# Optimization experiments

Hardware: AMD Instinct MI355X
Metric: run time of the kernel (lower is better)

The kernel has to match this reference:

```python
import jax, jax.numpy as jnp
import numpy as np

B, SQ, SK, E, H = 2, 256, 512, 512, 256

def _lin_init(k, fan_in, fan_out):
    return jax.random.normal(k, (fan_in, fan_out), jnp.float32) / np.sqrt(fan_in)

def setup_inputs() -> dict:
    key = jax.random.key(0)
    ks = jax.random.split(key, 16)
    inp = {
        'query': jax.random.normal(ks[0], (B, SQ, E), jnp.float32),
        'key':   jax.random.normal(ks[1], (B, SK, E), jnp.float32),
        # encoders
        'Wqe': _lin_init(ks[2], E, H), 'bqe': jnp.zeros((H,), jnp.float32),
        'Wke': _lin_init(ks[3], E, H), 'bke': jnp.zeros((H,), jnp.float32),
        # importance predictor: Linear(2H,H) x1, Linear(H,H) x2, Linear(H,1)
        'W0': _lin_init(ks[4], 2 * H, H), 'b0': jnp.zeros((H,), jnp.float32),
        'W1': _lin_init(ks[5], H, H),     'b1': jnp.zeros((H,), jnp.float32),
        'W2': _lin_init(ks[6], H, H),     'b2': jnp.zeros((H,), jnp.float32),
        'Wf': _lin_init(ks[7], H, 1),     'bf': jnp.zeros((1,), jnp.float32),
        # variance estimator: Linear(2H,H), Linear(H,1), Softplus
        'Wv1': _lin_init(ks[8], 2 * H, H), 'bv1': jnp.zeros((H,), jnp.float32),
        'Wv2': _lin_init(ks[9], H, 1),     'bv2': jnp.zeros((1,), jnp.float32),
    }
    return inp

def reference(query, key, Wqe, bqe, Wke, bke, W0, b0, W1, b1, W2, b2, Wf, bf, Wv1, bv1, Wv2, bv2):
    # Encoders (dropout is identity at eval): [B,Sq,H] and [B,Sk,H]
    qf = jax.nn.relu(jnp.einsum('bqe,eh->bqh', query, Wqe) + bqe)
    kf = jax.nn.relu(jnp.einsum('bke,eh->bkh', key, Wke) + bke)

    # concat([qf, kf]) @ W == qf @ W[:H] + kf @ W[H:]; avoid materializing the 2H concat
    Hd = qf.shape[-1]
    # importance predictor, layer 0 over all (q,k) pairs -> [B,Sq,Sk,H]
    q_part = jnp.einsum('bqh,hd->bqd', qf, W0[:Hd])
    k_part = jnp.einsum('bkh,hd->bkd', kf, W0[Hd:])
    h = jax.nn.relu(q_part[:, :, None, :] + k_part[:, None, :, :] + b0)
    h = jax.nn.relu(jnp.einsum('bqkh,hd->bqkd', h, W1) + b1)
    h = jax.nn.relu(jnp.einsum('bqkh,hd->bqkd', h, W2) + b2)
    importance_logits = (jnp.einsum('bqkh,ho->bqko', h, Wf) + bf)[..., 0]  # [B,Sq,Sk]

    # variance estimator
    qv = jnp.einsum('bqh,hd->bqd', qf, Wv1[:Hd])
    kv = jnp.einsum('bkh,hd->bkd', kf, Wv1[Hd:])
    v = jax.nn.relu(qv[:, :, None, :] + kv[:, None, :, :] + bv1)
    variance = jax.nn.softplus((jnp.einsum('bqkh,ho->bqko', v, Wv2) + bv2)[..., 0])

    return importance_logits, variance
```

## Files before the change

kernel.cpp:

```cpp
#include <hip/hip_runtime.h>
#include <hip/hip_bf16.h>
#include <math.h>

typedef __attribute__((ext_vector_type(4))) float f32x4;
typedef __attribute__((ext_vector_type(8))) short short8;
typedef __attribute__((ext_vector_type(4))) short short4v;

#define H_DIM 256
#define SQ_DIM 256
#define SK_DIM 512
#define E_DIM 512
#define B_DIM 2

__global__ __launch_bounds__(256) void split_cast(const float* __restrict__ query,
                                                  const float* __restrict__ key,
                                                  __hip_bfloat16* __restrict__ A1)
{
    int gid = blockIdx.x * 256 + threadIdx.x;
    int m  = gid >> 7;
    int kq = gid & 127;
    const float* src = (m < 512) ? query + (size_t)m * 512
                                 : key + (size_t)(m - 512) * 512;
    f32x4 v = *(const f32x4*)(src + kq * 4);
    short4v hv, lv;
    #pragma unroll
    for (int j = 0; j < 4; ++j) {
        __hip_bfloat16 h = __float2bfloat16(v[j]);
        float lf = v[j] - __bfloat162float(h);
        __hip_bfloat16 l = __float2bfloat16(lf);
        hv[j] = __builtin_bit_cast(short, h);
        lv[j] = __builtin_bit_cast(short, l);
    }
    *(short4v*)(A1 + (size_t)m * 1024 + kq * 4) = hv;
    *(short4v*)(A1 + (size_t)m * 1024 + 512 + kq * 4) = lv;
}

__global__ __launch_bounds__(256) void transpose_split(
    const float* __restrict__ Wqe, const float* __restrict__ Wke,
    const float* __restrict__ W0,  const float* __restrict__ Wv1,
    const float* __restrict__ W1,  const float* __restrict__ W2,
    __hip_bfloat16* __restrict__ Benc, __hip_bfloat16* __restrict__ Bproj,
    __hip_bfloat16* __restrict__ W1T,  __hip_bfloat16* __restrict__ W2T)
{
    __shared__ float tile[64][65];
    const float* S = nullptr; __hip_bfloat16* D = nullptr; int KJ = 256;
    bool split = true;
    switch (blockIdx.y) {
        case 0: S = Wqe;             D = Benc;                          KJ = 512; break;
        case 1: S = Wke;             D = Benc + 256 * 1024;             KJ = 512; break;
        case 2: S = W0;              D = Bproj;                         KJ = 256; break;
        case 3: S = Wv1;             D = Bproj + 256 * 512;             KJ = 256; break;
        case 4: S = W0 + 256 * 256;  D = Bproj + 512 * 512;             KJ = 256; break;
        case 5: S = Wv1 + 256 * 256; D = Bproj + 512 * 512 + 256 * 512; KJ = 256; break;
        case 6: S = W1;              D = W1T;  KJ = 256; split = false; break;
        case 7: S = W2;              D = W2T;  KJ = 256; split = false; break;
    }
    const int dstStride = split ? 2 * KJ : KJ;
    const int ntile = 4 * (KJ >> 6);
    const int x = blockIdx.x;
    if (x >= ntile) return;
    const int tx = x & 3, ty = x >> 2;
    const int k0 = ty * 64, n0 = tx * 64;
    const int t = threadIdx.x;
    #pragma unroll
    for (int i = 0; i < 16; ++i) {
        int r = (t >> 6) + i * 4;
        int c = t & 63;
        tile[r][c] = S[(size_t)(k0 + r) * 256 + n0 + c];
    }
    __syncthreads();
    #pragma unroll
    for (int i = 0; i < 16; ++i) {
        int r = (t >> 6) + i * 4;
        int c = t & 63;
        float v = tile[c][r];
        __hip_bfloat16 h = __float2bfloat16(v);
        D[(size_t)(n0 + r) * dstStride + k0 + c] = h;
        if (split) {
            float lf = v - __bfloat162float(h);
            D[(size_t)(n0 + r) * dstStride + KJ + k0 + c] = __float2bfloat16(lf);
        }
    }
}

template<int KD, bool SPLIT_OUT>
__global__ __launch_bounds__(256) void gemm3(
    const __hip_bfloat16* __restrict__ Apl,
    const __hip_bfloat16* __restrict__ B0,
    const __hip_bfloat16* __restrict__ B1,
    const float* __restrict__ bias0, const float* __restrict__ bias1,
    __hip_bfloat16* __restrict__ outS,
    float* __restrict__ outF0, float* __restrict__ outF1)
{
    __shared__ char smem[32768];
    const int t = threadIdx.x, lane = t & 63, wave = t >> 6;
    const int wm = wave >> 1, wn = wave & 1;
    const int m0 = blockIdx.y * 64, n0 = blockIdx.x * 64;
    const __hip_bfloat16* Arow = Apl + (size_t)m0 * (2 * KD);
    const __hip_bfloat16* Brow = ((m0 < 512) ? B0 : B1) + (size_t)n0 * (2 * KD);

    auto stage = [&](int c) {
        char* wb = smem + ((c & 1) << 14);
        const int k0 = c * 32;
        #pragma unroll
        for (int i = 0; i < 4; ++i) {
            int u = wave * 64 + lane + i * 256;
            int r = u >> 2;
            int sl = (u & 3) ^ ((r >> 1) & 3);
            int isB = r >> 7;
            int rr = r & 127;
            const __hip_bfloat16* base = isB ? Brow : Arow;
            const __hip_bfloat16* gp = base + (size_t)(rr >> 1) * (2 * KD)
                                       + (rr & 1) * KD + k0 + sl * 8;
            char* lp = wb + (wave * 64 + i * 256) * 16;
            __builtin_amdgcn_global_load_lds((const void*)gp, (void*)lp, 16, 0, 0);
        }
    };

    stage(0);
    __syncthreads();
    f32x4 acc[2][2];
    #pragma unroll
    for (int i = 0; i < 2; ++i)
        #pragma unroll
        for (int j = 0; j < 2; ++j) acc[i][j] = 0.f;

    const int NCH = KD / 32;
    for (int c = 0; c < NCH; ++c) {
        if (c + 1 < NCH) stage(c + 1);
        const char* wb = smem + ((c & 1) << 14);
        short8 ah[2], al[2];
        #pragma unroll
        for (int nt = 0; nt < 2; ++nt) {
            int n = wn * 32 + nt * 16 + (lane & 15);
            int rh = 128 + 2 * n, rl = rh + 1;
            ah[nt] = *(const short8*)(wb + rh * 64 + (((lane >> 4) ^ ((rh >> 1) & 3)) << 4));
            al[nt] = *(const short8*)(wb + rl * 64 + (((lane >> 4) ^ ((rl >> 1) & 3)) << 4));
        }
        #pragma unroll
        for (int mt = 0; mt < 2; ++mt) {
            int m = wm * 32 + mt * 16 + (lane & 15);
            int rh = 2 * m, rl = rh + 1;
            short8 bh = *(const short8*)(wb + rh * 64 + (((lane >> 4) ^ ((rh >> 1) & 3)) << 4));
            short8 bl = *(const short8*)(wb + rl * 64 + (((lane >> 4) ^ ((rl >> 1) & 3)) << 4));
            #pragma unroll
            for (int nt = 0; nt < 2; ++nt) {
                acc[mt][nt] = __builtin_amdgcn_mfma_f32_16x16x32_bf16(ah[nt], bh, acc[mt][nt], 0, 0, 0);
                acc[mt][nt] = __builtin_amdgcn_mfma_f32_16x16x32_bf16(al[nt], bh, acc[mt][nt], 0, 0, 0);
                acc[mt][nt] = __builtin_amdgcn_mfma_f32_16x16x32_bf16(ah[nt], bl, acc[mt][nt], 0, 0, 0);
            }
        }
        __syncthreads();
    }

    #pragma unroll
    for (int mt = 0; mt < 2; ++mt) {
        int m = m0 + wm * 32 + mt * 16 + (lane & 15);
        #pragma unroll
        for (int nt = 0; nt < 2; ++nt) {
            int nb = n0 + wn * 32 + nt * 16 + ((lane >> 4) << 2);
            if (SPLIT_OUT) {
                const float* bias = (m0 < 512) ? bias0 : bias1;
                f32x4 bv = *(const f32x4*)(bias + nb);
                short4v hv, lv;
                #pragma unroll
                for (int j = 0; j < 4; ++j) {
                    float v = fmaxf(acc[mt][nt][j] + bv[j], 0.f);
                    __hip_bfloat16 h = __float2bfloat16(v);
                    float lf = v - __bfloat162float(h);
                    hv[j] = __builtin_bit_cast(short, h);
                    lv[j] = __builtin_bit_cast(short, __float2bfloat16(lf));
                }
                *(short4v*)(outS + (size_t)m * 512 + nb) = hv;
                *(short4v*)(outS + (size_t)m * 512 + 256 + nb) = lv;
            } else {
                float* o = (nb < 256) ? outF0 + (size_t)m * 256 + nb
                                      : outF1 + (size_t)m * 256 + (nb - 256);
                *(f32x4*)o = acc[mt][nt];
            }
        }
    }
}

__global__ __launch_bounds__(512, 2) void pair_main(
    const float* __restrict__ qp, const float* __restrict__ kp,
    const float* __restrict__ qv, const float* __restrict__ kv,
    const __hip_bfloat16* __restrict__ W1T, const __hip_bfloat16* __restrict__ W2T,
    const float* __restrict__ b0, const float* __restrict__ b1,
    const float* __restrict__ b2, const float* __restrict__ Wf,
    const float* __restrict__ bf_, const float* __restrict__ bv1,
    const float* __restrict__ Wv2, const float* __restrict__ bv2,
    float* __restrict__ out)
{
    extern __shared__ char smem[];
    char* hbuf  = smem;
    char* wbuf0 = smem + 65536;
    char* wbuf1 = smem + 81920;

    const int t    = threadIdx.x;
    const int lane = t & 63, wave = t >> 6;
    const int wm   = wave >> 2, wn = wave & 3;
    const int idx  = blockIdx.x;
    const int q    = idx >> 3;
    const int kt   = idx & 3;
    const int b    = (idx >> 2) & 1;
    const int k0g  = kt * 128;

    const float* qprow  = qp + (size_t)(b * SQ_DIM + q) * H_DIM;
    const float* kprows = kp + (size_t)(b * SK_DIM + k0g) * H_DIM;

    auto stage = [&](int g) {
        const __hip_bfloat16* Wsrc = (g < 8) ? W1T : W2T;
        char* wb = (g & 1) ? wbuf1 : wbuf0;
        const int k0 = (g & 7) * 32;
        #pragma unroll
        for (int i = 0; i < 2; ++i) {
            int u = wave * 64 + i * 512 + lane;
            int n = u >> 2;
            int s_log = (u & 3) ^ ((n >> 1) & 3);
            const __hip_bfloat16* gp = Wsrc + n * H_DIM + k0 + s_log * 8;
            char* lp = wb + (wave * 64 + i * 512) * 16;
            __builtin_amdgcn_global_load_lds((const void*)gp, (void*)lp, 16, 0, 0);
        }
    };

    stage(0);

    #pragma unroll
    for (int i = 0; i < 8; ++i) {
        int cidx = t + 512 * i;
        int row  = cidx >> 5;
        int c8   = cidx & 31;
        const float* kr = kprows + row * H_DIM + c8 * 8;
        f32x4 k0v = *(const f32x4*)(kr);
        f32x4 k1v = *(const f32x4*)(kr + 4);
        f32x4 q0v = *(const f32x4*)(qprow + c8 * 8);
        f32x4 q1v = *(const f32x4*)(qprow + c8 * 8 + 4);
        f32x4 z0  = *(const f32x4*)(b0 + c8 * 8);
        f32x4 z1  = *(const f32x4*)(b0 + c8 * 8 + 4);
        short8 pk;
        #pragma unroll
        for (int j = 0; j < 4; ++j) {
            float v = fmaxf(k0v[j] + q0v[j] + z0[j], 0.f);
            float w = fmaxf(k1v[j] + q1v[j] + z1[j], 0.f);
            __hip_bfloat16 hv = __float2bfloat16(v);
            __hip_bfloat16 hw = __float2bfloat16(w);
            pk[j]     = __builtin_bit_cast(short, hv);
            pk[j + 4] = __builtin_bit_cast(short, hw);
        }
        int addr = (row * 512 + c8 * 16) ^ ((row & 7) << 4);
        *(short8*)(hbuf + addr) = pk;
    }
    __syncthreads();

    f32x4 acc[4][4];
    #pragma unroll
    for (int i = 0; i < 4; ++i)
        #pragma unroll
        for (int j = 0; j < 4; ++j)
            acc[i][j] = 0.f;

    auto gchunk = [&](int g) {
        const int c = g & 7;
        const char* wb = (g & 1) ? wbuf1 : wbuf0;
        if (g + 1 < 16) stage(g + 1);
        short8 afrag[4];
        #pragma unroll
        for (int nt = 0; nt < 4; ++nt) {
            int n = 64 * wn + 16 * nt + (lane & 15);
            int s_lds = (lane >> 4) ^ ((n >> 1) & 3);
            afrag[nt] = *(const short8*)(wb + n * 64 + s_lds * 16);
        }
        #pragma unroll
        for (int mt = 0; mt < 4; ++mt) {
            int m = 64 * wm + 16 * mt + (lane & 15);
            int addr = (m * 512 + c * 64 + ((lane >> 4) * 16)) ^ ((m & 7) << 4);
            short8 bfrag = *(const short8*)(hbuf + addr);
            #pragma unroll
            for (int nt = 0; nt < 4; ++nt)
                acc[mt][nt] = __builtin_amdgcn_mfma_f32_16x16x32_bf16(afrag[nt], bfrag, acc[mt][nt], 0, 0, 0);
        }
        __syncthreads();
    };

    for (int g = 0; g < 8; ++g)
        gchunk(g);

    #pragma unroll
    for (int mt = 0; mt < 4; ++mt) {
        int m = 64 * wm + 16 * mt + (lane & 15);
        #pragma unroll
        for (int nt = 0; nt < 4; ++nt) {
            int n0_ = 64 * wn + 16 * nt + ((lane >> 4) << 2);
            f32x4 bias = *(const f32x4*)(b1 + n0_);
            short4v pk;
            #pragma unroll
            for (int j = 0; j < 4; ++j) {
                float v = fmaxf(acc[mt][nt][j] + bias[j], 0.f);
                __hip_bfloat16 hv = __float2bfloat16(v);
                pk[j] = __builtin_bit_cast(short, hv);
            }
            int addr = (m * 512 + n0_ * 2) ^ ((m & 7) << 4);
            *(short4v*)(hbuf + addr) = pk;
            acc[mt][nt] = 0.f;
        }
    }
    __syncthreads();

    for (int g = 8; g < 16; ++g)
        gchunk(g);

    float p[4];
    #pragma unroll
    for (int mt = 0; mt < 4; ++mt) {
        float s = 0.f;
        #pragma unroll
        for (int nt = 0; nt < 4; ++nt) {
            int n0_ = 64 * wn + 16 * nt + ((lane >> 4) << 2);
            f32x4 wf   = *(const f32x4*)(Wf + n0_);
            f32x4 bias = *(const f32x4*)(b2 + n0_);
            #pragma unroll
            for (int j = 0; j < 4; ++j)
                s += fmaxf(acc[mt][nt][j] + bias[j], 0.f) * wf[j];
        }
        s += __shfl_xor(s, 16);
        s += __shfl_xor(s, 32);
        p[mt] = s;
    }

    float* lpart = (float*)smem;
    if (lane < 16) {
        #pragma unroll
        for (int mt = 0; mt < 4; ++mt)
            lpart[(wm * 64 + mt * 16 + lane) * 4 + wn] = p[mt];
    }
    __syncthreads();

    const size_t obase = (size_t)(b * SQ_DIM + q) * SK_DIM + k0g;
    if (t < 128) {
        f32x4 v = *(const f32x4*)(lpart + t * 4);
        out[obase + t] = v[0] + v[1] + v[2] + v[3] + bf_[0];
    }

    {
        int r = t >> 2, s4 = t & 3;
        const float* qvrow = qv + (size_t)(b * SQ_DIM + q) * H_DIM;
        const float* kvrow = kv + (size_t)(b * SK_DIM + k0g + r) * H_DIM;
        float a = 0.f;
        #pragma unroll
        for (int i = 0; i < 16; ++i) {
            int cidx = s4 * 64 + i * 4;
            f32x4 x  = *(const f32x4*)(qvrow + cidx);
            f32x4 y  = *(const f32x4*)(kvrow + cidx);
            f32x4 bb = *(const f32x4*)(bv1 + cidx);
            f32x4 wv = *(const f32x4*)(Wv2 + cidx);
            #pragma unroll
            for (int j = 0; j < 4; ++j)
                a += fmaxf(x[j] + y[j] + bb[j], 0.f) * wv[j];
        }
        a += __shfl_xor(a, 1);
        a += __shfl_xor(a, 2);
        if (s4 == 0) {
            float xx = a + bv2[0];
            float sp = (xx > 20.f) ? xx : log1pf(expf(xx));
            out[(size_t)B_DIM * SQ_DIM * SK_DIM + obase + r] = sp;
        }
    }
}

extern "C" void kernel_launch(void* const* d_in, const int* in_sizes, int n_in,
                              void* d_out, int out_size, void* d_ws, size_t ws_size,
                              hipStream_t stream)
{
    (void)in_sizes; (void)n_in; (void)out_size; (void)ws_size;

    const float* query = (const float*)d_in[0];
    const float* key   = (const float*)d_in[1];
    const float* Wqe   = (const float*)d_in[2];
    const float* bqe   = (const float*)d_in[3];
    const float* Wke   = (const float*)d_in[4];
    const float* bke   = (const float*)d_in[5];
    const float* W0    = (const float*)d_in[6];
    const float* b0    = (const float*)d_in[7];
    const float* W1    = (const float*)d_in[8];
    const float* b1    = (const float*)d_in[9];
    const float* W2    = (const float*)d_in[10];
    const float* b2    = (const float*)d_in[11];
    const float* Wf    = (const float*)d_in[12];
    const float* bf    = (const float*)d_in[13];
    const float* Wv1   = (const float*)d_in[14];
    const float* bv1   = (const float*)d_in[15];
    const float* Wv2   = (const float*)d_in[16];
    const float* bv2   = (const float*)d_in[17];
    float* out = (float*)d_out;

    char* ws = (char*)d_ws;
    __hip_bfloat16* A1    = (__hip_bfloat16*)(ws);
    __hip_bfloat16* Aq    = (__hip_bfloat16*)(ws + 3145728);
    __hip_bfloat16* Benc  = (__hip_bfloat16*)(ws + 4718592);
    __hip_bfloat16* Bproj = (__hip_bfloat16*)(ws + 5767168);
    __hip_bfloat16* W1T   = (__hip_bfloat16*)(ws + 6815744);
    __hip_bfloat16* W2T   = (__hip_bfloat16*)(ws + 6946816);
    float* qpkp = (float*)(ws);
    float* qvkv = (float*)(ws + 1572864);

    const float* qp = qpkp;
    const float* kp = qpkp + 512 * 256;
    const float* qv = qvkv;
    const float* kv = qvkv + 512 * 256;

    (void)hipFuncSetAttribute((const void*)pair_main,
                              hipFuncAttributeMaxDynamicSharedMemorySize, 98304);

    transpose_split<<<dim3(32, 8), 256, 0, stream>>>(Wqe, Wke, W0, Wv1, W1, W2,
                                                     Benc, Bproj, W1T, W2T);
    split_cast<<<dim3(768), 256, 0, stream>>>(query, key, A1);
    gemm3<512, true><<<dim3(4, 24), 256, 0, stream>>>(
        A1, Benc, Benc + 256 * 1024, bqe, bke, Aq, nullptr, nullptr);
    gemm3<256, false><<<dim3(8, 24), 256, 0, stream>>>(
        Aq, Bproj, Bproj + 512 * 512, nullptr, nullptr, nullptr, qpkp, qvkv);
    pair_main<<<dim3(2048), 512, 98304, stream>>>(qp, kp, qv, kv, W1T, W2T,
                                                  b0, b1, b2, Wf, bf, bv1, Wv2, bv2, out);
}
```

Before: 308.3 us.

## Triple-buffer weight staging with prefetch distance two and explicit waitcnt barriers

The pair kernel now streams W1T/W2T chunks into three rotating LDS buffers instead of two, issuing the load for chunk g+2 while chunk g is being computed. The full __syncthreads calls are replaced by targeted s_waitcnt vmcnt/lgkmcnt instructions plus raw s_barrier, so each wave waits only for the older chunk's loads. The chunk loops are unrolled so the buffer index is a compile-time constant. This aims to hide global-to-LDS latency behind the MFMA work. The cost is 16 KB more LDS per block and reliance on hand-counted vmcnt values being correct.

```diff
diff --git a/kernel.cpp b/kernel.cpp
--- a/kernel.cpp
+++ b/kernel.cpp
@@ -11,6 +11,15 @@
 #define SK_DIM 512
 #define E_DIM 512
 #define B_DIM 2
+
+#define RAW_BARRIER()  __builtin_amdgcn_s_barrier()
+#define SCHED_FENCE()  __builtin_amdgcn_sched_barrier(0)
+#define WAIT_VMCNT_2() do { asm volatile("s_waitcnt vmcnt(2)" ::: "memory"); \
+                            __builtin_amdgcn_sched_barrier(0); } while (0)
+#define WAIT_VMCNT_0() do { asm volatile("s_waitcnt vmcnt(0)" ::: "memory"); \
+                            __builtin_amdgcn_sched_barrier(0); } while (0)
+#define WAIT_LGKM_0()  do { asm volatile("s_waitcnt lgkmcnt(0)" ::: "memory"); \
+                            __builtin_amdgcn_sched_barrier(0); } while (0)
 
 __global__ __launch_bounds__(256) void split_cast(const float* __restrict__ query,
                                                   const float* __restrict__ key,
@@ -193,9 +202,8 @@
     float* __restrict__ out)
 {
     extern __shared__ char smem[];
-    char* hbuf  = smem;
-    char* wbuf0 = smem + 65536;
-    char* wbuf1 = smem + 81920;
+    char* hbuf = smem;
+    char* wbufs = smem + 65536;
 
     const int t    = threadIdx.x;
     const int lane = t & 63, wave = t >> 6;
@@ -211,7 +219,7 @@
 
     auto stage = [&](int g) {
         const __hip_bfloat16* Wsrc = (g < 8) ? W1T : W2T;
-        char* wb = (g & 1) ? wbuf1 : wbuf0;
+        char* wb = wbufs + (size_t)(g % 3) * 16384;
         const int k0 = (g & 7) * 32;
         #pragma unroll
         for (int i = 0; i < 2; ++i) {
@@ -223,8 +231,6 @@
             __builtin_amdgcn_global_load_lds((const void*)gp, (void*)lp, 16, 0, 0);
         }
     };
-
-    stage(0);
 
     #pragma unroll
     for (int i = 0; i < 8; ++i) {
@@ -251,7 +257,12 @@
         int addr = (row * 512 + c8 * 16) ^ ((row & 7) << 4);
         *(short8*)(hbuf + addr) = pk;
     }
-    __syncthreads();
+    stage(0);
+    stage(1);
+    SCHED_FENCE();
+    WAIT_VMCNT_2();
+    WAIT_LGKM_0();
+    RAW_BARRIER();
 
     f32x4 acc[4][4];
     #pragma unroll
@@ -260,10 +271,9 @@
         for (int j = 0; j < 4; ++j)
             acc[i][j] = 0.f;
 
-    auto gchunk = [&](int g) {
+    auto body = [&](int g) {
+        const char* wb = wbufs + (size_t)(g % 3) * 16384;
         const int c = g & 7;
-        const char* wb = (g & 1) ? wbuf1 : wbuf0;
-        if (g + 1 < 16) stage(g + 1);
         short8 afrag[4];
         #pragma unroll
         for (int nt = 0; nt < 4; ++nt) {
@@ -280,11 +290,17 @@
             for (int nt = 0; nt < 4; ++nt)
                 acc[mt][nt] = __builtin_amdgcn_mfma_f32_16x16x32_bf16(afrag[nt], bfrag, acc[mt][nt], 0, 0, 0);
         }
-        __syncthreads();
+        if (g + 2 < 16) stage(g + 2);
+        SCHED_FENCE();
+        if (g < 14) { WAIT_VMCNT_2(); }
+        else        { WAIT_VMCNT_0(); }
+        WAIT_LGKM_0();
+        RAW_BARRIER();
     };
 
+    #pragma unroll
     for (int g = 0; g < 8; ++g)
-        gchunk(g);
+        body(g);
 
     #pragma unroll
     for (int mt = 0; mt < 4; ++mt) {
@@ -305,10 +321,12 @@
             acc[mt][nt] = 0.f;
         }
     }
-    __syncthreads();
-
+    WAIT_LGKM_0();
+    RAW_BARRIER();
+
+    #pragma unroll
     for (int g = 8; g < 16; ++g)
-        gchunk(g);
+        body(g);
 
     float p[4];
     #pragma unroll
@@ -410,7 +428,7 @@
     const float* kv = qvkv + 512 * 256;
 
     (void)hipFuncSetAttribute((const void*)pair_main,
-                              hipFuncAttributeMaxDynamicSharedMemorySize, 98304);
+                              hipFuncAttributeMaxDynamicSharedMemorySize, 114688);
 
     transpose_split<<<dim3(32, 8), 256, 0, stream>>>(Wqe, Wke, W0, Wv1, W1, W2,
                                                      Benc, Bproj, W1T, W2T);
@@ -419,6 +437,6 @@
         A1, Benc, Benc + 256 * 1024, bqe, bke, Aq, nullptr, nullptr);
     gemm3<256, false><<<dim3(8, 24), 256, 0, stream>>>(
         Aq, Bproj, Bproj + 512 * 512, nullptr, nullptr, nullptr, qpkp, qvkv);
-    pair_main<<<dim3(2048), 512, 98304, stream>>>(qp, kp, qv, kv, W1T, W2T,
-                                                  b0, b1, b2, Wf, bf, bv1, Wv2, bv2, out);
+    pair_main<<<dim3(2048), 512, 114688, stream>>>(qp, kp, qv, kv, W1T, W2T,
+                                                   b0, b1, b2, Wf, bf, bv1, Wv2, bv2, out);
 }
```

Result: no change. 306.5 us (-0.6%).
